# Kernel optimization log

Hardware: AMD Instinct MI355X
Metric: run time of the kernel (lower is better)

Reference implementation:

```python
import jax, jax.numpy as jnp
import numpy as np

DIM = 64  # per-head dim, matches init_kwargs; dropout is identity in eval mode


def setup_inputs() -> dict:
    key = jax.random.key(0)
    kq, kk, kv = jax.random.split(key, 3)
    B, S, D = 16, 2048, DIM
    return {
        "query": jax.random.normal(kq, (B, S, D), dtype=jnp.float32),
        "key": jax.random.normal(kk, (B, S, D), dtype=jnp.float32),
        "value": jax.random.normal(kv, (B, S, D), dtype=jnp.float32),
    }


def reference(query, key, value):
    # score = Q K^T / sqrt(D)  -> [B, Sq, Sk]
    scale = 1.0 / np.sqrt(DIM).astype(np.float32)
    score = jnp.einsum("bqd,bkd->bqk", query, key) * scale
    attn = jax.nn.softmax(score, axis=-1)
    # dropout omitted (eval mode / p effectively identity for reference numerics)
    context = jnp.einsum("bqk,bkd->bqd", attn, value)
    return (context, attn)
```

## Files before the change

### kernel.cpp

```cpp
#include <hip/hip_runtime.h>
#include <hip/hip_bf16.h>

#define BATCH 16
#define SEQ   2048
#define DIM   64
#define CTX_ELEMS (BATCH * SEQ * DIM)
#define C_EXP2 0.18033688011112042f

typedef __attribute__((ext_vector_type(8))) __bf16 bf16x8;
typedef __attribute__((ext_vector_type(4))) __bf16 bf16x4;
typedef __attribute__((ext_vector_type(4))) float f32x4;

__global__ void convert_k(const float* __restrict__ K, __bf16* __restrict__ Kb) {
    int i = blockIdx.x * 256 + threadIdx.x;
    const float4* K4 = (const float4*)K;
    float4 v = K4[i];
    bf16x4 o;
    o[0] = (__bf16)v.x; o[1] = (__bf16)v.y; o[2] = (__bf16)v.z; o[3] = (__bf16)v.w;
    ((bf16x4*)Kb)[i] = o;
}

__global__ void trans_v(const float* __restrict__ V, __bf16* __restrict__ Vt) {
    __shared__ float tile[64][65];
    int b  = blockIdx.x >> 5;
    int kb = (blockIdx.x & 31) * 64;
    int t  = threadIdx.x;
    const float4* V4 = (const float4*)(V + ((size_t)(b * SEQ + kb)) * DIM);
    int d4 = (t & 15) * 4;
#pragma unroll
    for (int r = 0; r < 4; ++r) {
        int k = (t >> 4) + r * 16;
        float4 v = V4[k * (DIM / 4) + (t & 15)];
        tile[k][d4 + 0] = v.x; tile[k][d4 + 1] = v.y;
        tile[k][d4 + 2] = v.z; tile[k][d4 + 3] = v.w;
    }
    __syncthreads();
    int d  = t >> 2;
    int kl = (t & 3) * 16;
    bf16x8 v0, v1;
#pragma unroll
    for (int j = 0; j < 8; ++j) {
        v0[j] = (__bf16)tile[kl + j][d];
        v1[j] = (__bf16)tile[kl + 8 + j][d];
    }
    bf16x8* outv = (bf16x8*)(Vt + ((size_t)(b * DIM + d)) * SEQ + kb + kl);
    outv[0] = v0;
    outv[1] = v1;
}

__global__ __launch_bounds__(256, 8)
void attn_main(const float* __restrict__ Q, const __bf16* __restrict__ Kb,
               const __bf16* __restrict__ Vt, float* __restrict__ out) {
    __shared__ __bf16 plds[4][16][40];
    __shared__ float  redl[4][16];
    __shared__ float  ctxred[4][16][65];

    const int tid   = threadIdx.x;
    const int wave  = tid >> 6;
    const int lane  = tid & 63;
    const int quad  = lane >> 4;
    const int l16   = lane & 15;
    const int b     = blockIdx.y;
    const int qbase = blockIdx.x * 16;
    const int kbase = wave * (SEQ / 4);

    const float* qrow = Q + ((size_t)(b * SEQ + qbase + l16)) * DIM + quad * 8;
    bf16x8 aQ0, aQ1;
#pragma unroll
    for (int j = 0; j < 8; ++j) {
        aQ0[j] = (__bf16)qrow[j];
        aQ1[j] = (__bf16)qrow[32 + j];
    }

    const bf16x8* Kv = (const bf16x8*)(Kb + (size_t)b * SEQ * DIM);
    const bf16x8* Vv = (const bf16x8*)(Vt + (size_t)b * DIM * SEQ);

    float lsum = 0.f;
    for (int kt = 0; kt < SEQ / 64; ++kt) {
        int row = kbase + kt * 16 + l16;
        bf16x8 k0 = Kv[row * 8 + quad];
        bf16x8 k1 = Kv[row * 8 + quad + 4];
        f32x4 acc = {0.f, 0.f, 0.f, 0.f};
        acc = __builtin_amdgcn_mfma_f32_16x16x32_bf16(k0, aQ0, acc, 0, 0, 0);
        acc = __builtin_amdgcn_mfma_f32_16x16x32_bf16(k1, aQ1, acc, 0, 0, 0);
#pragma unroll
        for (int r = 0; r < 4; ++r)
            lsum += __builtin_amdgcn_exp2f(acc[r] * C_EXP2);
    }
    lsum += __shfl_xor(lsum, 16, 64);
    lsum += __shfl_xor(lsum, 32, 64);
    if (lane < 16) redl[wave][lane] = lsum;
    __syncthreads();
    const float rinv = 1.0f / (redl[0][l16] + redl[1][l16] + redl[2][l16] + redl[3][l16]);

    float* attn = out + CTX_ELEMS + (size_t)b * SEQ * SEQ
                + (size_t)(qbase + l16) * SEQ + kbase;
    f32x4 ctx[4];
#pragma unroll
    for (int nt = 0; nt < 4; ++nt) ctx[nt] = (f32x4){0.f, 0.f, 0.f, 0.f};
    const int vbase = kbase / 8;

    for (int ch = 0; ch < SEQ / 128; ++ch) {
#pragma unroll
        for (int half = 0; half < 2; ++half) {
            int kt  = ch * 2 + half;
            int row = kbase + kt * 16 + l16;
            bf16x8 k0 = Kv[row * 8 + quad];
            bf16x8 k1 = Kv[row * 8 + quad + 4];
            f32x4 acc = {0.f, 0.f, 0.f, 0.f};
            acc = __builtin_amdgcn_mfma_f32_16x16x32_bf16(k0, aQ0, acc, 0, 0, 0);
            acc = __builtin_amdgcn_mfma_f32_16x16x32_bf16(k1, aQ1, acc, 0, 0, 0);
            float4 pv;
            bf16x4 pb;
            {
                float p0 = __builtin_amdgcn_exp2f(acc[0] * C_EXP2) * rinv;
                float p1 = __builtin_amdgcn_exp2f(acc[1] * C_EXP2) * rinv;
                float p2 = __builtin_amdgcn_exp2f(acc[2] * C_EXP2) * rinv;
                float p3 = __builtin_amdgcn_exp2f(acc[3] * C_EXP2) * rinv;
                pv.x = p0; pv.y = p1; pv.z = p2; pv.w = p3;
                pb[0] = (__bf16)p0; pb[1] = (__bf16)p1;
                pb[2] = (__bf16)p2; pb[3] = (__bf16)p3;
            }
            *(float4*)(attn + kt * 16 + quad * 4) = pv;
            *(bf16x4*)&plds[wave][l16][half * 16 + quad * 4] = pb;
        }
        bf16x8 aP = *(const bf16x8*)&plds[wave][l16][quad * 8];
#pragma unroll
        for (int nt = 0; nt < 4; ++nt) {
            bf16x8 bv = Vv[(nt * 16 + l16) * (SEQ / 8) + vbase + ch * 4 + quad];
            ctx[nt] = __builtin_amdgcn_mfma_f32_16x16x32_bf16(aP, bv, ctx[nt], 0, 0, 0);
        }
    }

#pragma unroll
    for (int nt = 0; nt < 4; ++nt)
#pragma unroll
        for (int r = 0; r < 4; ++r)
            ctxred[wave][quad * 4 + r][nt * 16 + l16] = ctx[nt][r];
    __syncthreads();
    float* ctxout = out + ((size_t)(b * SEQ + qbase)) * DIM;
    for (int i = tid; i < 16 * DIM; i += 256) {
        int q = i >> 6, d = i & 63;
        ctxout[i] = ctxred[0][q][d] + ctxred[1][q][d] + ctxred[2][q][d] + ctxred[3][q][d];
    }
}

__global__ void attn_slow(const float* __restrict__ Q, const float* __restrict__ K,
                          const float* __restrict__ V, float* __restrict__ out) {
    __shared__ float sc[SEQ];
    __shared__ float qs[DIM];
    __shared__ float red[256];
    int b = blockIdx.y, q = blockIdx.x, t = threadIdx.x;
    const float* qp = Q + ((size_t)(b * SEQ + q)) * DIM;
    if (t < DIM) qs[t] = qp[t];
    __syncthreads();
    for (int k = t; k < SEQ; k += 256) {
        const float* kp = K + ((size_t)(b * SEQ + k)) * DIM;
        float s = 0.f;
        for (int d = 0; d < DIM; ++d) s += qs[d] * kp[d];
        sc[k] = __builtin_amdgcn_exp2f(s * C_EXP2);
    }
    __syncthreads();
    float part = 0.f;
    for (int k = t; k < SEQ; k += 256) part += sc[k];
#pragma unroll
    for (int m = 1; m < 64; m <<= 1) part += __shfl_xor(part, m, 64);
    if ((t & 63) == 0) red[t >> 6] = part;
    __syncthreads();
    float rinv = 1.0f / (red[0] + red[1] + red[2] + red[3]);
    float* attn = out + CTX_ELEMS + ((size_t)b * SEQ + q) * SEQ;
    for (int k = t; k < SEQ; k += 256) attn[k] = sc[k] * rinv;
    int d = t & 63, seg = t >> 6;
    float acc = 0.f;
    for (int k = seg * (SEQ / 4); k < (seg + 1) * (SEQ / 4); ++k)
        acc += sc[k] * V[((size_t)(b * SEQ + k)) * DIM + d];
    __syncthreads();
    red[t] = acc * rinv;
    __syncthreads();
    if (t < 64)
        out[((size_t)(b * SEQ + q)) * DIM + t] = red[t] + red[t + 64] + red[t + 128] + red[t + 192];
}

extern "C" void kernel_launch(void* const* d_in, const int* in_sizes, int n_in,
                              void* d_out, int out_size, void* d_ws, size_t ws_size,
                              hipStream_t stream) {
    const float* Q = (const float*)d_in[0];
    const float* K = (const float*)d_in[1];
    const float* V = (const float*)d_in[2];
    float* out = (float*)d_out;

    size_t need = (size_t)2 * BATCH * SEQ * DIM * sizeof(__bf16);
    if (ws_size >= need) {
        __bf16* Kb = (__bf16*)d_ws;
        __bf16* Vt = Kb + (size_t)BATCH * SEQ * DIM;
        convert_k<<<(BATCH * SEQ * DIM) / (256 * 4), 256, 0, stream>>>(K, Kb);
        trans_v<<<BATCH * (SEQ / 64), 256, 0, stream>>>(V, Vt);
        attn_main<<<dim3(SEQ / 16, BATCH), 256, 0, stream>>>(Q, Kb, Vt, out);
    } else {
        attn_slow<<<dim3(SEQ, BATCH), 256, 0, stream>>>(Q, K, V, out);
    }
}
```

Measured before the change: 435.0 us.

## Cache exp scores in registers, split keys over 8 waves, nontemporal attn stores

The block now runs 8 waves, each handling 256 keys instead of 512, so every wave's exponentiated scores (16 f32x4) can stay in registers. This removes the second QK^T MFMA pass and the second K reload. The attention matrix writes use nontemporal stores to avoid polluting cache. The cost is more register pressure, fewer blocks resident per CU, and a wider cross-wave reduction in LDS.

```diff
diff --git a/kernel.cpp b/kernel.cpp
--- a/kernel.cpp
+++ b/kernel.cpp
@@ -48,12 +48,12 @@
     outv[1] = v1;
 }
 
-__global__ __launch_bounds__(256, 8)
+__global__ __launch_bounds__(512, 4)
 void attn_main(const float* __restrict__ Q, const __bf16* __restrict__ Kb,
                const __bf16* __restrict__ Vt, float* __restrict__ out) {
-    __shared__ __bf16 plds[4][16][40];
-    __shared__ float  redl[4][16];
-    __shared__ float  ctxred[4][16][65];
+    __shared__ __bf16 plds[8][16][40];
+    __shared__ float  redl[8][16];
+    __shared__ float  ctxred[8][16][65];
 
     const int tid   = threadIdx.x;
     const int wave  = tid >> 6;
@@ -62,7 +62,7 @@
     const int l16   = lane & 15;
     const int b     = blockIdx.y;
     const int qbase = blockIdx.x * 16;
-    const int kbase = wave * (SEQ / 4);
+    const int kbase = wave * (SEQ / 8);
 
     const float* qrow = Q + ((size_t)(b * SEQ + qbase + l16)) * DIM + quad * 8;
     bf16x8 aQ0, aQ1;
@@ -75,23 +75,32 @@
     const bf16x8* Kv = (const bf16x8*)(Kb + (size_t)b * SEQ * DIM);
     const bf16x8* Vv = (const bf16x8*)(Vt + (size_t)b * DIM * SEQ);
 
+    f32x4 p[16];
     float lsum = 0.f;
-    for (int kt = 0; kt < SEQ / 64; ++kt) {
+#pragma unroll
+    for (int kt = 0; kt < 16; ++kt) {
         int row = kbase + kt * 16 + l16;
         bf16x8 k0 = Kv[row * 8 + quad];
         bf16x8 k1 = Kv[row * 8 + quad + 4];
         f32x4 acc = {0.f, 0.f, 0.f, 0.f};
         acc = __builtin_amdgcn_mfma_f32_16x16x32_bf16(k0, aQ0, acc, 0, 0, 0);
         acc = __builtin_amdgcn_mfma_f32_16x16x32_bf16(k1, aQ1, acc, 0, 0, 0);
-#pragma unroll
-        for (int r = 0; r < 4; ++r)
-            lsum += __builtin_amdgcn_exp2f(acc[r] * C_EXP2);
+        f32x4 e;
+#pragma unroll
+        for (int r = 0; r < 4; ++r) {
+            e[r] = __builtin_amdgcn_exp2f(acc[r] * C_EXP2);
+            lsum += e[r];
+        }
+        p[kt] = e;
     }
     lsum += __shfl_xor(lsum, 16, 64);
     lsum += __shfl_xor(lsum, 32, 64);
     if (lane < 16) redl[wave][lane] = lsum;
     __syncthreads();
-    const float rinv = 1.0f / (redl[0][l16] + redl[1][l16] + redl[2][l16] + redl[3][l16]);
+    float tot = 0.f;
+#pragma unroll
+    for (int w = 0; w < 8; ++w) tot += redl[w][l16];
+    const float rinv = 1.0f / tot;
 
     float* attn = out + CTX_ELEMS + (size_t)b * SEQ * SEQ
                 + (size_t)(qbase + l16) * SEQ + kbase;
@@ -100,28 +109,16 @@
     for (int nt = 0; nt < 4; ++nt) ctx[nt] = (f32x4){0.f, 0.f, 0.f, 0.f};
     const int vbase = kbase / 8;
 
-    for (int ch = 0; ch < SEQ / 128; ++ch) {
+#pragma unroll
+    for (int ch = 0; ch < 8; ++ch) {
 #pragma unroll
         for (int half = 0; half < 2; ++half) {
-            int kt  = ch * 2 + half;
-            int row = kbase + kt * 16 + l16;
-            bf16x8 k0 = Kv[row * 8 + quad];
-            bf16x8 k1 = Kv[row * 8 + quad + 4];
-            f32x4 acc = {0.f, 0.f, 0.f, 0.f};
-            acc = __builtin_amdgcn_mfma_f32_16x16x32_bf16(k0, aQ0, acc, 0, 0, 0);
-            acc = __builtin_amdgcn_mfma_f32_16x16x32_bf16(k1, aQ1, acc, 0, 0, 0);
-            float4 pv;
+            const int kt = ch * 2 + half;
+            f32x4 pn = p[kt] * rinv;
+            __builtin_nontemporal_store(pn, (f32x4*)(attn + kt * 16 + quad * 4));
             bf16x4 pb;
-            {
-                float p0 = __builtin_amdgcn_exp2f(acc[0] * C_EXP2) * rinv;
-                float p1 = __builtin_amdgcn_exp2f(acc[1] * C_EXP2) * rinv;
-                float p2 = __builtin_amdgcn_exp2f(acc[2] * C_EXP2) * rinv;
-                float p3 = __builtin_amdgcn_exp2f(acc[3] * C_EXP2) * rinv;
-                pv.x = p0; pv.y = p1; pv.z = p2; pv.w = p3;
-                pb[0] = (__bf16)p0; pb[1] = (__bf16)p1;
-                pb[2] = (__bf16)p2; pb[3] = (__bf16)p3;
-            }
-            *(float4*)(attn + kt * 16 + quad * 4) = pv;
+            pb[0] = (__bf16)pn[0]; pb[1] = (__bf16)pn[1];
+            pb[2] = (__bf16)pn[2]; pb[3] = (__bf16)pn[3];
             *(bf16x4*)&plds[wave][l16][half * 16 + quad * 4] = pb;
         }
         bf16x8 aP = *(const bf16x8*)&plds[wave][l16][quad * 8];
@@ -139,9 +136,12 @@
             ctxred[wave][quad * 4 + r][nt * 16 + l16] = ctx[nt][r];
     __syncthreads();
     float* ctxout = out + ((size_t)(b * SEQ + qbase)) * DIM;
-    for (int i = tid; i < 16 * DIM; i += 256) {
+    for (int i = tid; i < 16 * DIM; i += 512) {
         int q = i >> 6, d = i & 63;
-        ctxout[i] = ctxred[0][q][d] + ctxred[1][q][d] + ctxred[2][q][d] + ctxred[3][q][d];
+        float s = 0.f;
+#pragma unroll
+        for (int w = 0; w < 8; ++w) s += ctxred[w][q][d];
+        ctxout[i] = s;
     }
 }
 
@@ -195,7 +195,7 @@
         __bf16* Vt = Kb + (size_t)BATCH * SEQ * DIM;
         convert_k<<<(BATCH * SEQ * DIM) / (256 * 4), 256, 0, stream>>>(K, Kb);
         trans_v<<<BATCH * (SEQ / 64), 256, 0, stream>>>(V, Vt);
-        attn_main<<<dim3(SEQ / 16, BATCH), 256, 0, stream>>>(Q, Kb, Vt, out);
+        attn_main<<<dim3(SEQ / 16, BATCH), 512, 0, stream>>>(Q, Kb, Vt, out);
     } else {
         attn_slow<<<dim3(SEQ, BATCH), 256, 0, stream>>>(Q, K, V, out);
     }
```

New measurement: 399.7 us. 8.1% less time.
